# Performance work log

Hardware: AMD Instinct MI355X
Metric: run time of the kernel (lower is better)

The kernel has to match this reference:

```python
import math
import jax, jax.numpy as jnp
import numpy as np

L, B, N, D, H, DFF = 4, 64, 511, 256, 8, 512
S = N + 1          # +1 game token
HD = D // H
BW = 7             # BOARD_WIDTH (undefined global in source; board-game policy width)


def layer_norm(x, g, b):
    m = jnp.mean(x, axis=-1, keepdims=True)
    v = jnp.var(x, axis=-1, keepdims=True)
    return (x - m) / jnp.sqrt(v + 1e-5) * g + b


def setup_inputs() -> dict:
    key = jax.random.key(0)
    ks = jax.random.split(key, 24)

    def p(k, shape):
        return jax.random.normal(k, shape, jnp.float32) * 0.02

    return {
        "cell_states": jax.random.randint(ks[0], (B * N,), 0, 3, dtype=jnp.int32),
        "edge_type_matrix": jax.random.randint(ks[1], (B, N, N), 0, 3, dtype=jnp.int32),
        "patch_emb": p(ks[2], (3, D)),
        "game_token": p(ks[3], (1, 1, D)),
        "edge_emb": p(ks[4], (3, H)),   # zeros in source init; random here to exercise bias path
        "in_w": p(ks[5], (L, 3 * D, D)), "in_b": p(ks[6], (L, 3 * D)),
        "out_w": p(ks[7], (L, D, D)), "out_b": p(ks[8], (L, D)),
        "ff1_w": p(ks[9], (L, DFF, D)), "ff1_b": p(ks[10], (L, DFF)),
        "ff2_w": p(ks[11], (L, D, DFF)), "ff2_b": p(ks[12], (L, D)),
        "ln1_g": jnp.ones((L, D)), "ln1_b": jnp.zeros((L, D)),
        "ln2_g": jnp.ones((L, D)), "ln2_b": jnp.zeros((L, D)),
        "fc1_w": p(ks[13], (64, D)), "fc1_b": p(ks[14], (64,)),
        "pol_w": p(ks[15], (BW, 64)), "pol_b": p(ks[16], (BW,)),
        "val_w": p(ks[17], (1, 64)), "val_b": p(ks[18], (1,)),
    }


def reference(cell_states, edge_type_matrix, patch_emb, game_token, edge_emb,
              in_w, in_b, out_w, out_b, ff1_w, ff1_b, ff2_w, ff2_b,
              ln1_g, ln1_b, ln2_g, ln2_b, fc1_w, fc1_b, pol_w, pol_b, val_w, val_b):
    # embed cells and prepend game token -> [B, S, D]
    x = patch_emb[cell_states].reshape(B, N, D)
    x = jnp.concatenate([jnp.broadcast_to(game_token, (B, 1, D)), x], axis=1)

    # edge bias: [B,N,N,H] -> [B,H,N,N], pad token row/col with zeros -> [B,H,S,S]
    bias = jnp.transpose(edge_emb[edge_type_matrix], (0, 3, 1, 2))
    bias = jnp.pad(bias, ((0, 0), (0, 0), (1, 0), (1, 0)))

    scale = math.sqrt(HD)
    for i in range(L):
        h = layer_norm(x, ln1_g[i], ln1_b[i])
        qkv = h @ in_w[i].T + in_b[i]                       # [B,S,3D]
        q, k, v = jnp.split(qkv, 3, axis=-1)
        q = q.reshape(B, S, H, HD).transpose(0, 2, 1, 3)    # [B,H,S,HD]
        k = k.reshape(B, S, H, HD).transpose(0, 2, 1, 3)
        v = v.reshape(B, S, H, HD).transpose(0, 2, 1, 3)
        scores = jnp.einsum('bhqd,bhkd->bhqk', q, k) / scale + bias
        attn = jax.nn.softmax(scores, axis=-1)              # dropout = identity (eval)
        o = jnp.einsum('bhqk,bhkd->bhqd', attn, v)
        o = o.transpose(0, 2, 1, 3).reshape(B, S, D)
        x = x + (o @ out_w[i].T + out_b[i])
        h2 = layer_norm(x, ln2_g[i], ln2_b[i])
        x = x + (jax.nn.relu(h2 @ ff1_w[i].T + ff1_b[i]) @ ff2_w[i].T + ff2_b[i])

    g = x[:, 0, :]
    o = jax.nn.relu(g @ fc1_w.T + fc1_b)
    policy_logits = o @ pol_w.T + pol_b
    value = jnp.tanh(o @ val_w.T + val_b)
    return policy_logits, value
```

## Files before the change

### kernel.cpp

```cpp
#include <hip/hip_runtime.h>
#include <hip/hip_bf16.h>
#include <math.h>

#define L_ 4
#define B_ 64
#define N_ 511
#define D_ 256
#define H_ 8
#define DFF_ 512
#define S_ 512
#define HD_ 32
#define BW_ 7
#define BS_ (B_*S_)

typedef __attribute__((ext_vector_type(8))) short short8;
typedef __attribute__((ext_vector_type(4))) short short4v;
typedef __attribute__((ext_vector_type(4))) float f32x4;

#define L2E 1.44269504088896340f
#define QSCL (0.17677669529663687f * 1.44269504088896340f)

#if defined(__HIP_DEVICE_COMPILE__) && __has_builtin(__builtin_amdgcn_exp2f)
#define EXP2(x) __builtin_amdgcn_exp2f(x)
#else
#define EXP2(x) exp2f(x)
#endif

__device__ inline ushort f2b(float f) {
    unsigned u = __float_as_uint(f);
    unsigned r = (u + 0x7fffu + ((u >> 16) & 1u)) >> 16;
    return (ushort)r;
}

#if defined(__HIP_DEVICE_COMPILE__) && __has_builtin(__builtin_amdgcn_cvt_pk_bf16_f32)
typedef __attribute__((ext_vector_type(2))) __bf16 bf16x2_t;
__device__ inline uint pk_bf16(float a, float b) {
    bf16x2_t r = __builtin_amdgcn_cvt_pk_bf16_f32(a, b);
    return *(uint*)&r;
}
#else
__device__ inline uint pk_bf16(float a, float b) {
    return (uint)f2b(a) | ((uint)f2b(b) << 16);
}
#endif

__device__ inline f32x4 bsel4v(uint E, uint tlo, uint thi) {
    f32x4 r;
#if defined(__HIP_DEVICE_COMPILE__) && __has_builtin(__builtin_amdgcn_perm)
    uint E2  = E + E;
    uint E2b = E2 | 0x01010101u;
    uint s01 = __builtin_amdgcn_perm(E2b, E2, 0x05010400u);
    uint s23 = __builtin_amdgcn_perm(E2b, E2, 0x07030602u);
    uint p01 = __builtin_amdgcn_perm(thi, tlo, s01);
    uint p23 = __builtin_amdgcn_perm(thi, tlo, s23);
    r[0] = __uint_as_float(p01 << 16);
    r[1] = __uint_as_float(p01 & 0xFFFF0000u);
    r[2] = __uint_as_float(p23 << 16);
    r[3] = __uint_as_float(p23 & 0xFFFF0000u);
#else
    #pragma unroll
    for (int i = 0; i < 4; i++) {
        unsigned char e = (unsigned char)((E >> (8 * i)) & 0xff);
        uint bb = e == 0 ? (tlo & 0xFFFFu) : (e == 1 ? (tlo >> 16) :
                  (e == 2 ? (thi & 0xFFFFu) : 0u));
        r[i] = __uint_as_float(bb << 16);
    }
#endif
    return r;
}

__device__ inline void gload16(const void* g, void* l) {
#if __has_builtin(__builtin_amdgcn_global_load_lds)
    __builtin_amdgcn_global_load_lds(
        (const __attribute__((address_space(1))) void*)g,
        (__attribute__((address_space(3))) void*)l, 16, 0, 0);
#else
    *(short8*)l = *(const short8*)g;
#endif
}

__global__ __launch_bounds__(256) void build_ln(const int* __restrict__ cs,
                                                const float* __restrict__ patch,
                                                const float* __restrict__ game,
                                                const float* __restrict__ gw,
                                                const float* __restrict__ bw,
                                                float* __restrict__ x,
                                                ushort* __restrict__ h)
{
    int t = threadIdx.x;
    int lane = t & 63;
    int wv = t >> 6;
    int row = blockIdx.x * 4 + wv;
    int s = row & (S_ - 1);
    float4 v;
    if (s == 0) {
        v = ((const float4*)game)[lane];
    } else {
        int b = row >> 9;
        int cell = cs[b * N_ + s - 1];
        v = ((const float4*)(patch + cell * D_))[lane];
    }
    ((float4*)x)[(size_t)row * 64 + lane] = v;

    float sm = v.x + v.y + v.z + v.w;
    #pragma unroll
    for (int o = 32; o >= 1; o >>= 1) sm += __shfl_xor(sm, o);
    float mean = sm * (1.f / 256.f);
    float dx = v.x - mean, dy = v.y - mean, dz = v.z - mean, dw = v.w - mean;
    float s2 = dx * dx + dy * dy + dz * dz + dw * dw;
    #pragma unroll
    for (int o = 32; o >= 1; o >>= 1) s2 += __shfl_xor(s2, o);
    float rstd = rsqrtf(s2 * (1.f / 256.f) + 1e-5f);
    float4 g  = *(const float4*)(gw + lane * 4);
    float4 bb = *(const float4*)(bw + lane * 4);
    ushort4 o4;
    o4.x = f2b(dx * rstd * g.x + bb.x);
    o4.y = f2b(dy * rstd * g.y + bb.y);
    o4.z = f2b(dz * rstd * g.z + bb.z);
    o4.w = f2b(dw * rstd * g.w + bb.w);
    *(ushort4*)(h + (size_t)row * D_ + lane * 4) = o4;
}

__global__ __launch_bounds__(256) void build_et8(const int* __restrict__ et,
                                                 unsigned char* __restrict__ et8)
{
    long idx = (long)blockIdx.x * 256 + threadIdx.x;
    int k = (int)(idx & (S_ - 1));
    long rem = idx >> 9;
    int q = (int)(rem & (S_ - 1));
    int b = (int)(rem >> 9);
    unsigned char v = 3;
    if (q > 0 && k > 0) {
        v = (unsigned char)et[((long)b * N_ + (q - 1)) * N_ + (k - 1)];
    }
    et8[idx] = v;
}

__global__ __launch_bounds__(256) void convert_all(const float* __restrict__ in_w,
                                                   const float* __restrict__ out_w,
                                                   const float* __restrict__ ff1_w,
                                                   const float* __restrict__ ff2_w,
                                                   ushort* __restrict__ inwb,
                                                   ushort* __restrict__ outwb,
                                                   ushort* __restrict__ ff1wb,
                                                   ushort* __restrict__ ff2wb)
{
    int i = blockIdx.x * 256 + threadIdx.x;
    const float* src;
    ushort* dst;
    int j;
    float s = 1.f;
    if (i < 196608) {
        j = i; src = in_w; dst = inwb;
        int r = (j >> 6) % 768;
        if (r < 256) s = (float)QSCL;
    } else if (i < 262144) {
        j = i - 196608; src = out_w; dst = outwb;
    } else if (i < 393216) {
        j = i - 262144; src = ff1_w; dst = ff1wb;
    } else {
        j = i - 393216; src = ff2_w; dst = ff2wb;
    }
    float4 v = ((const float4*)src)[j];
    ushort4 o4;
    o4.x = f2b(v.x * s); o4.y = f2b(v.y * s); o4.z = f2b(v.z * s); o4.w = f2b(v.w * s);
    ((ushort4*)dst)[j] = o4;
}

template<int K, int NT, bool RELU, bool QSC, bool QKV>
__global__ __launch_bounds__(256, 2) void gemm_lds(const ushort* __restrict__ A,
                                                   const ushort* __restrict__ W,
                                                   const float* __restrict__ bias,
                                                   ushort* __restrict__ Cout,
                                                   ushort* __restrict__ Kb,
                                                   ushort* __restrict__ Vt)
{
    __shared__ ushort As[2][4096];
    __shared__ ushort Ws[2][4096];
    const int N = NT * 128;
    int t = threadIdx.x;
    int wave = t >> 6, lane = t & 63;
    int lr = lane & 15, quad = lane >> 4;
    int lk = quad * 8;
    int blk = blockIdx.x;
    int xcd = blk & 7, idx = blk >> 3;
    int m0 = (xcd * 32 + (idx & 31)) * 128;
    int n0 = (idx >> 5) * 128;
    int mh = (wave >> 1) * 64, nh = (wave & 1) * 64;

    const ushort* ga0 = A + (size_t)(m0 + (t >> 2)) * K + (t & 3) * 8;
    const ushort* ga1 = ga0 + (size_t)64 * K;
    const ushort* gw0 = W + (size_t)(n0 + (t >> 2)) * K + (t & 3) * 8;
    const ushort* gw1 = gw0 + (size_t)64 * K;
    int t8 = t * 8;

    f32x4 acc[4][4];
    f32x4 zz = {0.f, 0.f, 0.f, 0.f};
    #pragma unroll
    for (int i = 0; i < 4; i++)
        #pragma unroll
        for (int j = 0; j < 4; j++) acc[i][j] = zz;

    for (int k0 = 0; k0 < K; k0 += 64) {
        gload16(ga0 + k0,      &As[0][t8]);
        gload16(ga1 + k0,      &As[0][t8 + 2048]);
        gload16(ga0 + k0 + 32, &As[1][t8]);
        gload16(ga1 + k0 + 32, &As[1][t8 + 2048]);
        gload16(gw0 + k0,      &Ws[0][t8]);
        gload16(gw1 + k0,      &Ws[0][t8 + 2048]);
        gload16(gw0 + k0 + 32, &Ws[1][t8]);
        gload16(gw1 + k0 + 32, &Ws[1][t8 + 2048]);
        __syncthreads();
        short8 af[2][4], wf[2][4];
        #pragma unroll
        for (int kk = 0; kk < 2; kk++) {
            #pragma unroll
            for (int i = 0; i < 4; i++) af[kk][i] = *(const short8*)&As[kk][(mh + i * 16 + lr) * 32 + lk];
            #pragma unroll
            for (int j = 0; j < 4; j++) wf[kk][j] = *(const short8*)&Ws[kk][(nh + j * 16 + lr) * 32 + lk];
        }
        #pragma unroll
        for (int kk = 0; kk < 2; kk++)
            #pragma unroll
            for (int i = 0; i < 4; i++)
                #pragma unroll
                for (int j = 0; j < 4; j++)
                    acc[i][j] = __builtin_amdgcn_mfma_f32_16x16x32_bf16(af[kk][i], wf[kk][j], acc[i][j], 0, 0, 0);
        __syncthreads();
    }

    #pragma unroll
    for (int nt = 0; nt < 4; nt++) {
        int colbase = n0 + nh + nt * 16;
        int col = colbase + lr;
        float bv = bias[col];
        if (QSC && colbase < 256) bv *= (float)QSCL;
        int region = QKV ? (colbase >> 8) : 0;
        #pragma unroll
        for (int mt = 0; mt < 4; mt++) {
            int rowb = m0 + mh + mt * 16 + quad * 4;
            if (!QKV || region == 0) {
                #pragma unroll
                for (int r = 0; r < 4; r++) {
                    size_t cidx = (size_t)(rowb + r) * N + col;
                    float v = acc[mt][nt][r] + bv;
                    if (RELU) v = fmaxf(v, 0.f);
                    Cout[cidx] = f2b(v);
                }
            } else if (region == 1) {
                int hh = (col >> 5) & 7, d = col & 31;
                int bb = rowb >> 9, s = rowb & 511;
                size_t kbase = ((size_t)(bb * 8 + hh) * 512 + s) * 32 + d;
                #pragma unroll
                for (int r = 0; r < 4; r++)
                    Kb[kbase + (size_t)r * 32] = f2b(acc[mt][nt][r] + bv);
            } else {
                int hh = (col >> 5) & 7, d = col & 31;
                int bb = rowb >> 9, s = rowb & 511;
                ushort4 w;
                w.x = f2b(acc[mt][nt][0] + bv);
                w.y = f2b(acc[mt][nt][1] + bv);
                w.z = f2b(acc[mt][nt][2] + bv);
                w.w = f2b(acc[mt][nt][3] + bv);
                size_t vidx = (((size_t)(bb * 8 + hh) * 32 + (s >> 4)) * 32 + d) * 16 + (s & 15);
                *(ushort4*)&Vt[vidx] = w;
            }
        }
    }
}

template<int K>
__global__ __launch_bounds__(256, 2) void gemm_ln(const ushort* __restrict__ A,
                                                  const ushort* __restrict__ W,
                                                  const float* __restrict__ bias,
                                                  float* __restrict__ X,
                                                  const float* __restrict__ lng,
                                                  const float* __restrict__ lnb,
                                                  ushort* __restrict__ Hout)
{
    __shared__ ushort As[2][2048];
    __shared__ ushort Ws[2][8192];
    __shared__ float lds_s[64][4];
    __shared__ float lds_q[64][4];
    int t = threadIdx.x;
    int wave = t >> 6, lane = t & 63;
    int lr = lane & 15, quad = lane >> 4;
    int lk = quad * 8;
    int blk = blockIdx.x;
    int xcd = blk & 7;
    int m0 = (xcd * 64 + (blk >> 3)) * 64;
    int nh = wave * 64;

    const ushort* ga = A + (size_t)(m0 + (t >> 2)) * K + (t & 3) * 8;
    const ushort* gw = W + (size_t)(t >> 2) * K + (t & 3) * 8;
    int t8 = t * 8;

    f32x4 acc[4][4];
    f32x4 zz = {0.f, 0.f, 0.f, 0.f};
    #pragma unroll
    for (int i = 0; i < 4; i++)
        #pragma unroll
        for (int j = 0; j < 4; j++) acc[i][j] = zz;

    for (int k0 = 0; k0 < K; k0 += 64) {
        gload16(ga + k0,      &As[0][t8]);
        gload16(ga + k0 + 32, &As[1][t8]);
        #pragma unroll
        for (int j = 0; j < 4; j++) {
            gload16(gw + (size_t)(j * 64) * K + k0,      &Ws[0][t8 + j * 2048]);
            gload16(gw + (size_t)(j * 64) * K + k0 + 32, &Ws[1][t8 + j * 2048]);
        }
        __syncthreads();
        short8 af[2][4], wf[2][4];
        #pragma unroll
        for (int kk = 0; kk < 2; kk++) {
            #pragma unroll
            for (int i = 0; i < 4; i++) af[kk][i] = *(const short8*)&As[kk][(i * 16 + lr) * 32 + lk];
            #pragma unroll
            for (int j = 0; j < 4; j++) wf[kk][j] = *(const short8*)&Ws[kk][(nh + j * 16 + lr) * 32 + lk];
        }
        #pragma unroll
        for (int kk = 0; kk < 2; kk++)
            #pragma unroll
            for (int i = 0; i < 4; i++)
                #pragma unroll
                for (int j = 0; j < 4; j++)
                    acc[i][j] = __builtin_amdgcn_mfma_f32_16x16x32_bf16(af[kk][i], wf[kk][j], acc[i][j], 0, 0, 0);
        __syncthreads();
    }

    float gc[4], bc[4], bi[4];
    #pragma unroll
    for (int nt = 0; nt < 4; nt++) {
        int col = nh + nt * 16 + lr;
        gc[nt] = lng[col]; bc[nt] = lnb[col]; bi[nt] = bias[col];
    }
    float psum[16], psq[16];
    #pragma unroll
    for (int e = 0; e < 16; e++) { psum[e] = 0.f; psq[e] = 0.f; }
    #pragma unroll
    for (int nt = 0; nt < 4; nt++) {
        #pragma unroll
        for (int mt = 0; mt < 4; mt++) {
            #pragma unroll
            for (int r = 0; r < 4; r++) {
                int row = m0 + mt * 16 + quad * 4 + r;
                size_t idx = (size_t)row * D_ + nh + nt * 16 + lr;
                float v = acc[mt][nt][r] + bi[nt] + X[idx];
                X[idx] = v;
                acc[mt][nt][r] = v;
                psum[mt * 4 + r] += v;
                psq[mt * 4 + r]  += v * v;
            }
        }
    }
    #pragma unroll
    for (int e = 0; e < 16; e++) {
        float s = psum[e], q = psq[e];
        s += __shfl_xor(s, 1); q += __shfl_xor(q, 1);
        s += __shfl_xor(s, 2); q += __shfl_xor(q, 2);
        s += __shfl_xor(s, 4); q += __shfl_xor(q, 4);
        s += __shfl_xor(s, 8); q += __shfl_xor(q, 8);
        psum[e] = s; psq[e] = q;
    }
    if (lr == 0) {
        #pragma unroll
        for (int mt = 0; mt < 4; mt++)
            #pragma unroll
            for (int r = 0; r < 4; r++) {
                int rl = mt * 16 + quad * 4 + r;
                lds_s[rl][wave] = psum[mt * 4 + r];
                lds_q[rl][wave] = psq[mt * 4 + r];
            }
    }
    __syncthreads();
    #pragma unroll
    for (int mt = 0; mt < 4; mt++) {
        #pragma unroll
        for (int r = 0; r < 4; r++) {
            int rl = mt * 16 + quad * 4 + r;
            f32x4 ss = *(const f32x4*)lds_s[rl];
            f32x4 qq = *(const f32x4*)lds_q[rl];
            float s = ss[0] + ss[1] + ss[2] + ss[3];
            float q = qq[0] + qq[1] + qq[2] + qq[3];
            float mean = s * (1.f / 256.f);
            float rstd = rsqrtf(q * (1.f / 256.f) - mean * mean + 1e-5f);
            int row = m0 + mt * 16 + quad * 4 + r;
            #pragma unroll
            for (int nt = 0; nt < 4; nt++) {
                size_t idx = (size_t)row * D_ + nh + nt * 16 + lr;
                float hv = (acc[mt][nt][r] - mean) * rstd * gc[nt] + bc[nt];
                Hout[idx] = f2b(hv);
            }
        }
    }
}

__global__ __launch_bounds__(256, 4) void attn_mfma(const ushort* __restrict__ qkv,
                                                    const ushort* __restrict__ Kb,
                                                    const ushort* __restrict__ Vt,
                                                    const unsigned char* __restrict__ et8,
                                                    const float* __restrict__ eemb,
                                                    ushort* __restrict__ o)
{
    int t = threadIdx.x;
    int wave = t >> 6, lane = t & 63;
    int lr = lane & 15, quad = lane >> 4;
    int lk = quad * 8;
    int blk = blockIdx.x;
    int b = ((blk >> 8) << 3) | (blk & 7);
    int h = (blk >> 3) & 7;
    int qq = (blk >> 6) & 3;
    int bh = b * 8 + h;
    int q0 = qq * 128 + wave * 32;
    float eb0 = eemb[h] * L2E, eb1 = eemb[8 + h] * L2E, eb2 = eemb[16 + h] * L2E;
    uint tlo = (uint)f2b(eb0) | ((uint)f2b(eb1) << 16);
    uint thi = (uint)f2b(eb2);

    short8 qf[2];
    #pragma unroll
    for (int X = 0; X < 2; X++)
        qf[X] = *(const short8*)(qkv + ((size_t)(b * S_ + q0 + X * 16 + lr)) * 768 + h * 32 + lk);
    int gl = ((lr >> 2) << 3) | (lr & 3);
    const ushort* Kp = Kb + ((size_t)(bh * S_) + gl) * 32 + lk;
    const ushort* Vp = Vt + (size_t)bh * 16384 + (quad >> 1) * 512 + lr * 16 + (quad & 1) * 8;
    const unsigned char* Ep0 = et8 + ((size_t)(b * S_ + q0 + lr)) * 512 + quad * 8;
    const unsigned char* Ep1 = Ep0 + (size_t)16 * 512;

    const short8 vones8 = { (short)0x3F80, (short)0x3F80, (short)0x3F80, (short)0x3F80,
                            (short)0x3F80, (short)0x3F80, (short)0x3F80, (short)0x3F80 };

    f32x4 zz = {0.f, 0.f, 0.f, 0.f};
    f32x4 oacc[2][2], lacc[2];
    #pragma unroll
    for (int X = 0; X < 2; X++) { oacc[X][0] = zz; oacc[X][1] = zz; lacc[X] = zz; }

    short8 kf0 = *(const short8*)(Kp);
    short8 kf1 = *(const short8*)(Kp + 128);
    uint2 e0 = *(const uint2*)(Ep0);
    uint2 e1 = *(const uint2*)(Ep1);
    short8 vb0 = *(const short8*)(Vp);
    short8 vb1 = *(const short8*)(Vp + 256);
    Kp += 1024; Ep0 += 32; Ep1 += 32; Vp += 1024;

    #pragma unroll 2
    for (int it = 0; it < 16; ++it) {
        short8 nk0 = *(const short8*)(Kp);
        short8 nk1 = *(const short8*)(Kp + 128);
        uint2 ne0 = *(const uint2*)(Ep0);
        uint2 ne1 = *(const uint2*)(Ep1);
        short8 nv0 = *(const short8*)(Vp);
        short8 nv1 = *(const short8*)(Vp + 256);
        Kp += 1024; Ep0 += 32; Ep1 += 32; Vp += 1024;
        #pragma unroll
        for (int X = 0; X < 2; X++) {
            uint Ea = X ? e1.x : e0.x;
            uint Eb = X ? e1.y : e0.y;
            f32x4 c0 = bsel4v(Ea, tlo, thi);
            f32x4 c1 = bsel4v(Eb, tlo, thi);
            f32x4 s0 = __builtin_amdgcn_mfma_f32_16x16x32_bf16(kf0, qf[X], c0, 0, 0, 0);
            f32x4 s1 = __builtin_amdgcn_mfma_f32_16x16x32_bf16(kf1, qf[X], c1, 0, 0, 0);
            float p0[4], p1[4];
            #pragma unroll
            for (int r = 0; r < 4; r++) {
                p0[r] = EXP2(s0[r]);
                p1[r] = EXP2(s1[r]);
            }
            union { short8 v; uint u[4]; } PA;
            PA.u[0] = pk_bf16(p0[0], p0[1]); PA.u[1] = pk_bf16(p0[2], p0[3]);
            PA.u[2] = pk_bf16(p1[0], p1[1]); PA.u[3] = pk_bf16(p1[2], p1[3]);
            oacc[X][0] = __builtin_amdgcn_mfma_f32_16x16x32_bf16(PA.v, vb0, oacc[X][0], 0, 0, 0);
            oacc[X][1] = __builtin_amdgcn_mfma_f32_16x16x32_bf16(PA.v, vb1, oacc[X][1], 0, 0, 0);
            lacc[X]    = __builtin_amdgcn_mfma_f32_16x16x32_bf16(PA.v, vones8, lacc[X], 0, 0, 0);
        }
        kf0 = nk0; kf1 = nk1; e0 = ne0; e1 = ne1; vb0 = nv0; vb1 = nv1;
    }

    #pragma unroll
    for (int X = 0; X < 2; X++) {
        #pragma unroll
        for (int r = 0; r < 4; r++) {
            int q = quad * 4 + r;
            float inv = 1.f / lacc[X][r];
            size_t base = (size_t)(b * S_ + q0 + X * 16 + q) * D_ + h * 32;
            o[base + lr]      = f2b(oacc[X][0][r] * inv);
            o[base + 16 + lr] = f2b(oacc[X][1][r] * inv);
        }
    }
}

__global__ __launch_bounds__(64) void head_kernel(const float* __restrict__ x,
                                                  const float* __restrict__ fc1w,
                                                  const float* __restrict__ fc1b,
                                                  const float* __restrict__ polw,
                                                  const float* __restrict__ polb,
                                                  const float* __restrict__ valw,
                                                  const float* __restrict__ valb,
                                                  float* __restrict__ out)
{
    __shared__ float o1[64];
    int b = blockIdx.x;
    int t = threadIdx.x;
    const float* g = x + (size_t)b * S_ * D_;
    float acc = fc1b[t];
    for (int k = 0; k < D_; k++) acc += g[k] * fc1w[t * D_ + k];
    o1[t] = fmaxf(acc, 0.f);
    __syncthreads();
    if (t < BW_) {
        float a = polb[t];
        for (int k = 0; k < 64; k++) a += o1[k] * polw[t * 64 + k];
        out[b * BW_ + t] = a;
    } else if (t == BW_) {
        float a = valb[0];
        for (int k = 0; k < 64; k++) a += o1[k] * valw[k];
        out[B_ * BW_ + b] = tanhf(a);
    }
}

extern "C" void kernel_launch(void* const* d_in, const int* in_sizes, int n_in,
                              void* d_out, int out_size, void* d_ws, size_t ws_size,
                              hipStream_t stream)
{
    const int*   cs    = (const int*)d_in[0];
    const int*   etm   = (const int*)d_in[1];
    const float* patch = (const float*)d_in[2];
    const float* game  = (const float*)d_in[3];
    const float* eemb  = (const float*)d_in[4];
    const float* in_w  = (const float*)d_in[5];
    const float* in_b  = (const float*)d_in[6];
    const float* out_w = (const float*)d_in[7];
    const float* out_b = (const float*)d_in[8];
    const float* ff1_w = (const float*)d_in[9];
    const float* ff1_b = (const float*)d_in[10];
    const float* ff2_w = (const float*)d_in[11];
    const float* ff2_b = (const float*)d_in[12];
    const float* ln1_g = (const float*)d_in[13];
    const float* ln1_b = (const float*)d_in[14];
    const float* ln2_g = (const float*)d_in[15];
    const float* ln2_b = (const float*)d_in[16];
    const float* fc1_w = (const float*)d_in[17];
    const float* fc1_b = (const float*)d_in[18];
    const float* pol_w = (const float*)d_in[19];
    const float* pol_b = (const float*)d_in[20];
    const float* val_w = (const float*)d_in[21];
    const float* val_b = (const float*)d_in[22];
    float* out = (float*)d_out;

    char* base = (char*)d_ws;
    float*  x     = (float*)(base + 0);
    ushort* h     = (ushort*)(base + 33554432);
    ushort* qkvb  = (ushort*)(base + 50331648);
    ushort* Kb    = (ushort*)(base + 100663296);
    ushort* Vt    = (ushort*)(base + 117440512);
    ushort* ob    = (ushort*)(base + 134217728);
    unsigned char* et8 = (unsigned char*)(base + 150994944);
    ushort* inwb  = (ushort*)(base + 167772160);
    ushort* outwb = (ushort*)(base + 169345024);
    ushort* ff1wb = (ushort*)(base + 169869312);
    ushort* ff2wb = (ushort*)(base + 170917888);

    build_et8<<<65536, 256, 0, stream>>>(etm, et8);
    convert_all<<<2048, 256, 0, stream>>>(in_w, out_w, ff1_w, ff2_w,
                                          inwb, outwb, ff1wb, ff2wb);
    build_ln<<<8192, 256, 0, stream>>>(cs, patch, game, ln1_g, ln1_b, x, h);

    for (int i = 0; i < L_; i++) {
        gemm_lds<256, 6, false, true, true><<<1536, 256, 0, stream>>>(
            h, inwb + (size_t)i * 196608, in_b + i * 768, qkvb, Kb, Vt);
        attn_mfma<<<2048, 256, 0, stream>>>(qkvb, Kb, Vt, et8, eemb, ob);
        gemm_ln<256><<<512, 256, 0, stream>>>(
            ob, outwb + (size_t)i * 65536, out_b + i * 256, x,
            ln2_g + i * D_, ln2_b + i * D_, h);
        gemm_lds<256, 4, true, false, false><<<1024, 256, 0, stream>>>(
            h, ff1wb + (size_t)i * 131072, ff1_b + i * 512, qkvb, nullptr, nullptr);
        int nx = (i + 1 < L_) ? (i + 1) : i;
        gemm_ln<512><<<512, 256, 0, stream>>>(
            qkvb, ff2wb + (size_t)i * 131072, ff2_b + i * 256, x,
            ln1_g + nx * D_, ln1_b + nx * D_, h);
    }
    head_kernel<<<B_, 64, 0, stream>>>(x, fc1_w, fc1_b, pol_w, pol_b, val_w, val_b, out);
}
```

Baseline: 771.3 us.

## Compute only game-token row in final layer after QKV projection

Measured after the change: 689.7 us. 10.6% less time.

```diff
diff --git a/kernel.cpp b/kernel.cpp
--- a/kernel.cpp
+++ b/kernel.cpp
@@ -30,6 +30,10 @@
     unsigned u = __float_as_uint(f);
     unsigned r = (u + 0x7fffu + ((u >> 16) & 1u)) >> 16;
     return (ushort)r;
+}
+
+__device__ inline float b2f(ushort u) {
+    return __uint_as_float(((uint)u) << 16);
 }
 
 #if defined(__HIP_DEVICE_COMPILE__) && __has_builtin(__builtin_amdgcn_cvt_pk_bf16_f32)
@@ -489,6 +493,124 @@
     }
 }
 
+__global__ __launch_bounds__(64) void attn_last(const ushort* __restrict__ qkv,
+                                                const ushort* __restrict__ Kb,
+                                                const ushort* __restrict__ Vt,
+                                                ushort* __restrict__ o)
+{
+    int lane = threadIdx.x;
+    int bh = blockIdx.x;
+    int b = bh >> 3, h = bh & 7;
+    __shared__ float ps[512];
+
+    const ushort* qp = qkv + (size_t)(b * S_) * 768 + h * 32;
+    float q[32];
+    #pragma unroll
+    for (int d8 = 0; d8 < 4; d8++) {
+        short8 v = *(const short8*)(qp + d8 * 8);
+        #pragma unroll
+        for (int j = 0; j < 8; j++) q[d8 * 8 + j] = b2f((ushort)v[j]);
+    }
+    const ushort* kp = Kb + ((size_t)bh * 512 + lane * 8) * 32;
+    float lsum = 0.f;
+    #pragma unroll
+    for (int j = 0; j < 8; j++) {
+        float s = 0.f;
+        #pragma unroll
+        for (int d8 = 0; d8 < 4; d8++) {
+            short8 kv = *(const short8*)(kp + j * 32 + d8 * 8);
+            #pragma unroll
+            for (int e = 0; e < 8; e++) s += q[d8 * 8 + e] * b2f((ushort)kv[e]);
+        }
+        float pe = b2f(f2b(EXP2(s)));
+        ps[lane * 8 + j] = pe;
+        lsum += pe;
+    }
+    #pragma unroll
+    for (int off = 32; off >= 1; off >>= 1) lsum += __shfl_xor(lsum, off);
+    __syncthreads();
+
+    int d = lane & 31, kh = lane >> 5;
+    const ushort* vp = Vt + (size_t)bh * 16384 + d * 16;
+    float acc = 0.f;
+    for (int k = kh * 256; k < kh * 256 + 256; k += 16) {
+        const ushort* vt = vp + (size_t)(k >> 4) * 512;
+        #pragma unroll
+        for (int e = 0; e < 16; e++) acc += ps[k + e] * b2f(vt[e]);
+    }
+    acc += __shfl_xor(acc, 32);
+    if (lane < 32)
+        o[(size_t)(b * S_) * D_ + h * 32 + d] = f2b(acc / lsum);
+}
+
+__global__ __launch_bounds__(256) void last_tail(const ushort* __restrict__ ob,
+                                                 const ushort* __restrict__ outw,
+                                                 const float* __restrict__ outb,
+                                                 const float* __restrict__ ln2g,
+                                                 const float* __restrict__ ln2b,
+                                                 const ushort* __restrict__ ff1w,
+                                                 const float* __restrict__ ff1b,
+                                                 const ushort* __restrict__ ff2w,
+                                                 const float* __restrict__ ff2b,
+                                                 float* __restrict__ X)
+{
+    __shared__ float obs[256];
+    __shared__ ushort h2s[256];
+    __shared__ ushort ffs[512];
+    __shared__ float red[8];
+    int t = threadIdx.x;
+    int b = blockIdx.x;
+    size_t row = (size_t)b * S_;
+
+    obs[t] = b2f(ob[row * D_ + t]);
+    __syncthreads();
+
+    const ushort* w0 = outw + (size_t)t * 256;
+    float acc = 0.f;
+    for (int k8 = 0; k8 < 256; k8 += 8) {
+        short8 wv = *(const short8*)(w0 + k8);
+        #pragma unroll
+        for (int e = 0; e < 8; e++) acc += obs[k8 + e] * b2f((ushort)wv[e]);
+    }
+    float xv = acc + outb[t] + X[row * D_ + t];
+
+    float s1 = xv, s2 = xv * xv;
+    #pragma unroll
+    for (int off = 32; off >= 1; off >>= 1) { s1 += __shfl_xor(s1, off); s2 += __shfl_xor(s2, off); }
+    int wv_ = t >> 6, lane = t & 63;
+    if (lane == 0) { red[wv_] = s1; red[4 + wv_] = s2; }
+    __syncthreads();
+    float S1 = red[0] + red[1] + red[2] + red[3];
+    float S2 = red[4] + red[5] + red[6] + red[7];
+    float mean = S1 * (1.f / 256.f);
+    float rstd = rsqrtf(S2 * (1.f / 256.f) - mean * mean + 1e-5f);
+    h2s[t] = f2b((xv - mean) * rstd * ln2g[t] + ln2b[t]);
+    __syncthreads();
+
+    #pragma unroll
+    for (int cc = 0; cc < 2; cc++) {
+        int col = t + cc * 256;
+        const ushort* w1 = ff1w + (size_t)col * 256;
+        float a = 0.f;
+        for (int k8 = 0; k8 < 256; k8 += 8) {
+            short8 wv1 = *(const short8*)(w1 + k8);
+            #pragma unroll
+            for (int e = 0; e < 8; e++) a += b2f(h2s[k8 + e]) * b2f((ushort)wv1[e]);
+        }
+        ffs[col] = f2b(fmaxf(a + ff1b[col], 0.f));
+    }
+    __syncthreads();
+
+    const ushort* w2 = ff2w + (size_t)t * 512;
+    float a2 = 0.f;
+    for (int k8 = 0; k8 < 512; k8 += 8) {
+        short8 wv2 = *(const short8*)(w2 + k8);
+        #pragma unroll
+        for (int e = 0; e < 8; e++) a2 += b2f(ffs[k8 + e]) * b2f((ushort)wv2[e]);
+    }
+    X[row * D_ + t] = a2 + ff2b[t] + xv;
+}
+
 __global__ __launch_bounds__(64) void head_kernel(const float* __restrict__ x,
                                                   const float* __restrict__ fc1w,
                                                   const float* __restrict__ fc1b,
@@ -567,16 +689,24 @@
     for (int i = 0; i < L_; i++) {
         gemm_lds<256, 6, false, true, true><<<1536, 256, 0, stream>>>(
             h, inwb + (size_t)i * 196608, in_b + i * 768, qkvb, Kb, Vt);
-        attn_mfma<<<2048, 256, 0, stream>>>(qkvb, Kb, Vt, et8, eemb, ob);
-        gemm_ln<256><<<512, 256, 0, stream>>>(
-            ob, outwb + (size_t)i * 65536, out_b + i * 256, x,
-            ln2_g + i * D_, ln2_b + i * D_, h);
-        gemm_lds<256, 4, true, false, false><<<1024, 256, 0, stream>>>(
-            h, ff1wb + (size_t)i * 131072, ff1_b + i * 512, qkvb, nullptr, nullptr);
-        int nx = (i + 1 < L_) ? (i + 1) : i;
-        gemm_ln<512><<<512, 256, 0, stream>>>(
-            qkvb, ff2wb + (size_t)i * 131072, ff2_b + i * 256, x,
-            ln1_g + nx * D_, ln1_b + nx * D_, h);
+        if (i < L_ - 1) {
+            attn_mfma<<<2048, 256, 0, stream>>>(qkvb, Kb, Vt, et8, eemb, ob);
+            gemm_ln<256><<<512, 256, 0, stream>>>(
+                ob, outwb + (size_t)i * 65536, out_b + i * 256, x,
+                ln2_g + i * D_, ln2_b + i * D_, h);
+            gemm_lds<256, 4, true, false, false><<<1024, 256, 0, stream>>>(
+                h, ff1wb + (size_t)i * 131072, ff1_b + i * 512, qkvb, nullptr, nullptr);
+            gemm_ln<512><<<512, 256, 0, stream>>>(
+                qkvb, ff2wb + (size_t)i * 131072, ff2_b + i * 256, x,
+                ln1_g + (i + 1) * D_, ln1_b + (i + 1) * D_, h);
+        } else {
+            attn_last<<<512, 64, 0, stream>>>(qkvb, Kb, Vt, ob);
+            last_tail<<<64, 256, 0, stream>>>(
+                ob, outwb + (size_t)i * 65536, out_b + i * 256,
+                ln2_g + i * D_, ln2_b + i * D_,
+                ff1wb + (size_t)i * 131072, ff1_b + i * 512,
+                ff2wb + (size_t)i * 131072, ff2_b + i * 256, x);
+        }
     }
     head_kernel<<<B_, 64, 0, stream>>>(x, fc1_w, fc1_b, pol_w, pol_b, val_w, val_b, out);
 }
```
